# Kernel tuning notes

Hardware: AMD Instinct MI355X
Metric: run time of the kernel (lower is better)

## Reference

```python
import jax, jax.numpy as jnp
import numpy as np

N_NODES = 50000
N_EDGES = 800000
IN_FEATS = 128
OUT_FEATS = 128


def setup_inputs() -> dict:
    key = jax.random.key(0)
    k1, k2, k3, k4, k5 = jax.random.split(key, 5)
    feat = jax.random.normal(k1, (N_NODES, IN_FEATS), dtype=jnp.float32)
    src = jax.random.randint(k2, (N_EDGES,), 0, N_NODES, dtype=jnp.int64)
    dst = jax.random.randint(k3, (N_EDGES,), 0, N_NODES, dtype=jnp.int64)
    # Glorot uniform weight, zero bias (as in reset_parameters)
    limit = float(np.sqrt(6.0 / (IN_FEATS + OUT_FEATS)))
    weight = jax.random.uniform(k4, (IN_FEATS, OUT_FEATS), dtype=jnp.float32,
                                minval=-limit, maxval=limit)
    bias = jnp.zeros((OUT_FEATS,), dtype=jnp.float32)
    return {"feat": feat, "src": src, "dst": dst, "weight": weight, "bias": bias}


def reference(feat, src, dst, weight, bias):
    ones = jnp.ones(src.shape[0], dtype=feat.dtype)
    # out-degree normalization on source side
    deg_out = jnp.maximum(jax.ops.segment_sum(ones, src, num_segments=N_NODES), 1.0)
    h = feat * (deg_out ** -0.5)[:, None]  # [N, in]
    # in_feats <= out_feats: aggregate first, then matmul
    agg = jax.ops.segment_sum(h[src], dst, num_segments=N_NODES)  # SpMM: [N, in]
    rst = jnp.matmul(agg, weight)  # [N, out]
    # in-degree normalization on destination side
    deg_in = jnp.maximum(jax.ops.segment_sum(ones, dst, num_segments=N_NODES), 1.0)
    rst = rst * (deg_in ** -0.5)[:, None]
    rst = rst + bias
    return rst
```

## Files before the change

### kernel.cpp

```cpp
#include <hip/hip_runtime.h>

#define IN_F 128
#define HRH 4
#define HCD 64
#define HCS 32
#define HRB 8
#define HIST_RS 12544
#define BIN_RS 6272
#define LROW 68

typedef __attribute__((ext_vector_type(8))) short bf16x8;
typedef __attribute__((ext_vector_type(4))) float f32x4;

static __device__ __forceinline__ unsigned short f2bf(float x) {
    unsigned u = __float_as_uint(x);
    unsigned r = (u + 0x7FFFu + ((u >> 16) & 1u)) >> 16;
    return (unsigned short)r;
}

#define RFL(x) __builtin_amdgcn_readfirstlane(x)

__global__ __launch_bounds__(256) void k_hist(const int* __restrict__ src,
                                              const int* __restrict__ dst,
                                              int* __restrict__ dstpart,
                                              int* __restrict__ srcpart,
                                              int nN, int nE) {
    __shared__ int h[HIST_RS];
    int bid = blockIdx.x;
    const int* key;
    int* part;
    int r, c, nch;
    if (bid < HRH * HCD) {
        key = dst; part = dstpart; nch = HCD;
        r = bid / HCD; c = bid % HCD;
    } else {
        bid -= HRH * HCD;
        key = src; part = srcpart; nch = HCS;
        r = bid / HCS; c = bid % HCS;
    }
    const int rs   = (nN + HRH - 1) / HRH;
    const int rbeg = r * rs;
    const int rsize = min(rs, nN - rbeg);
    if (rsize <= 0) return;

    for (int i = threadIdx.x; i < rsize; i += 256) h[i] = 0;
    __syncthreads();

    const int chunk = (nE + nch - 1) / nch;
    const int ebeg = c * chunk;
    const int eend = min(ebeg + chunk, nE);

    if ((ebeg & 3) == 0) {
        for (int i = ebeg + threadIdx.x * 4; i < eend; i += 256 * 4) {
            if (i + 3 < eend) {
                const int4 k4 = *reinterpret_cast<const int4*>(key + i);
                int a;
                a = k4.x - rbeg; if ((unsigned)a < (unsigned)rsize) atomicAdd(&h[a], 1);
                a = k4.y - rbeg; if ((unsigned)a < (unsigned)rsize) atomicAdd(&h[a], 1);
                a = k4.z - rbeg; if ((unsigned)a < (unsigned)rsize) atomicAdd(&h[a], 1);
                a = k4.w - rbeg; if ((unsigned)a < (unsigned)rsize) atomicAdd(&h[a], 1);
            } else {
                for (int j = i; j < eend; ++j) {
                    int a = key[j] - rbeg;
                    if ((unsigned)a < (unsigned)rsize) atomicAdd(&h[a], 1);
                }
            }
        }
    } else {
        for (int i = ebeg + threadIdx.x; i < eend; i += 256) {
            int a = key[i] - rbeg;
            if ((unsigned)a < (unsigned)rsize) atomicAdd(&h[a], 1);
        }
    }
    __syncthreads();

    int* pout = part + (size_t)c * nN + rbeg;
    for (int i = threadIdx.x; i < rsize; i += 256) pout[i] = h[i];
}

__global__ void k_merge(int* __restrict__ dstpart, const int* __restrict__ srcpart,
                        int* __restrict__ cnt_pad, int* __restrict__ creal,
                        float* __restrict__ dinv_out, float* __restrict__ dinv_in,
                        int nN) {
    const int n = blockIdx.x * blockDim.x + threadIdx.x;
    if (n > nN) return;
    if (n == nN) { cnt_pad[n] = 0; return; }
    int s = 0;
#pragma unroll 4
    for (int c = 0; c < HCS; ++c) s += srcpart[(size_t)c * nN + n];
    int run = 0;
#pragma unroll 4
    for (int c = 0; c < HCD; ++c) {
        const size_t idx = (size_t)c * nN + n;
        int v = dstpart[idx];
        dstpart[idx] = run;
        run += v;
    }
    cnt_pad[n]  = (run + 7) & ~7;
    creal[n]    = run;
    dinv_out[n] = rsqrtf(fmaxf((float)s, 1.0f));
    dinv_in[n]  = rsqrtf(fmaxf((float)run, 1.0f));
}

__global__ __launch_bounds__(256) void k_scan_blk(const int* __restrict__ cnt,
                                                  int* __restrict__ offs,
                                                  int* __restrict__ part, int nNs) {
    __shared__ int ts[256];
    const int t = threadIdx.x;
    const int base = blockIdx.x * 1024 + t * 4;
    int4 v = make_int4(0, 0, 0, 0);
    if (base + 3 < nNs) {
        v = *reinterpret_cast<const int4*>(cnt + base);
    } else {
        if (base + 0 < nNs) v.x = cnt[base + 0];
        if (base + 1 < nNs) v.y = cnt[base + 1];
        if (base + 2 < nNs) v.z = cnt[base + 2];
        if (base + 3 < nNs) v.w = cnt[base + 3];
    }
    const int s = v.x + v.y + v.z + v.w;
    ts[t] = s;
    __syncthreads();
    for (int d = 1; d < 256; d <<= 1) {
        int u = (t >= d) ? ts[t - d] : 0;
        __syncthreads();
        ts[t] += u;
        __syncthreads();
    }
    const int ex = ts[t] - s;
    if (t == 255) part[blockIdx.x] = ts[255];
    int4 o;
    o.x = ex;
    o.y = o.x + v.x;
    o.z = o.y + v.y;
    o.w = o.z + v.z;
    if (base + 3 < nNs) {
        *reinterpret_cast<int4*>(offs + base) = o;
    } else {
        if (base + 0 < nNs) offs[base + 0] = o.x;
        if (base + 1 < nNs) offs[base + 1] = o.y;
        if (base + 2 < nNs) offs[base + 2] = o.z;
        if (base + 3 < nNs) offs[base + 3] = o.w;
    }
}

__global__ __launch_bounds__(256) void k_scan_top(int* __restrict__ part, int nb) {
    __shared__ int ts[256];
    const int t = threadIdx.x;
    const int v = (t < nb) ? part[t] : 0;
    ts[t] = v;
    __syncthreads();
    for (int d = 1; d < 256; d <<= 1) {
        int u = (t >= d) ? ts[t - d] : 0;
        __syncthreads();
        ts[t] += u;
        __syncthreads();
    }
    if (t < nb) part[t] = ts[t] - v;
}

__global__ __launch_bounds__(256) void k_scan_add(int* __restrict__ offs,
                                                  const int* __restrict__ part,
                                                  int nNs) {
    const int base = blockIdx.x * 1024 + threadIdx.x * 4;
    const int add = part[blockIdx.x];
    if (base + 3 < nNs) {
        int4 o = *reinterpret_cast<int4*>(offs + base);
        o.x += add; o.y += add; o.z += add; o.w += add;
        *reinterpret_cast<int4*>(offs + base) = o;
    } else {
#pragma unroll
        for (int j = 0; j < 4; ++j)
            if (base + j < nNs) offs[base + j] += add;
    }
}

__global__ void k_pad(const int* __restrict__ offs, const int* __restrict__ creal,
                      int* __restrict__ eidx, int nN) {
    const int n = blockIdx.x * blockDim.x + threadIdx.x;
    if (n >= nN) return;
    const int s = offs[n] + creal[n];
    const int e = offs[n + 1];
    for (int i = s; i < e; ++i) eidx[i] = nN;
}

__global__ __launch_bounds__(256) void k_bin2(const int* __restrict__ src,
                                              const int* __restrict__ dst,
                                              const int* __restrict__ offs,
                                              const int* __restrict__ chunkoff,
                                              int* __restrict__ eidx, int nN, int nE) {
    __shared__ int cur[BIN_RS];
    const int bid = blockIdx.x;
    const int r = bid / HCD;
    const int c = bid % HCD;
    const int rs = (nN + HRB - 1) / HRB;
    const int rbeg = r * rs;
    const int rsize = min(rs, nN - rbeg);
    if (rsize <= 0) return;

    for (int i = threadIdx.x; i < rsize; i += 256)
        cur[i] = offs[rbeg + i] + chunkoff[(size_t)c * nN + rbeg + i];
    __syncthreads();

    const int chunk = (nE + HCD - 1) / HCD;
    const int ebeg = c * chunk;
    const int eend = min(ebeg + chunk, nE);
    for (int i = ebeg + threadIdx.x * 4; i < eend; i += 256 * 4) {
        if (i + 3 < eend) {
            const int4 d4 = *reinterpret_cast<const int4*>(dst + i);
            int d;
            d = d4.x - rbeg; if ((unsigned)d < (unsigned)rsize) { int p = atomicAdd(&cur[d], 1); eidx[p] = src[i + 0]; }
            d = d4.y - rbeg; if ((unsigned)d < (unsigned)rsize) { int p = atomicAdd(&cur[d], 1); eidx[p] = src[i + 1]; }
            d = d4.z - rbeg; if ((unsigned)d < (unsigned)rsize) { int p = atomicAdd(&cur[d], 1); eidx[p] = src[i + 2]; }
            d = d4.w - rbeg; if ((unsigned)d < (unsigned)rsize) { int p = atomicAdd(&cur[d], 1); eidx[p] = src[i + 3]; }
        } else {
            for (int j = i; j < eend; ++j) {
                int d = dst[j] - rbeg;
                if ((unsigned)d < (unsigned)rsize) { int p = atomicAdd(&cur[d], 1); eidx[p] = src[j]; }
            }
        }
    }
}

__global__ __launch_bounds__(256) void k_scale(const float* __restrict__ feat,
                                               const float* __restrict__ dinv,
                                               unsigned short* __restrict__ h, int nN) {
    const int i = blockIdx.x * 256 + threadIdx.x;
    if (i >= (nN + 1) * (IN_F / 4)) return;
    const int node = i >> 5;
    const int j = (i & 31) * 4;
    ushort4 o = make_ushort4(0, 0, 0, 0);
    if (node < nN) {
        const float s = dinv[node];
        const float4 v = *reinterpret_cast<const float4*>(feat + (size_t)node * IN_F + j);
        o.x = f2bf(v.x * s);
        o.y = f2bf(v.y * s);
        o.z = f2bf(v.z * s);
        o.w = f2bf(v.w * s);
    }
    *reinterpret_cast<ushort4*>(h + (size_t)node * IN_F + j) = o;
}

__global__ __launch_bounds__(256) void k_wprep(const float* __restrict__ W,
                                               unsigned short* __restrict__ wt) {
    __shared__ float wl[128 * 128];
    for (int i = threadIdx.x * 4; i < 128 * 128; i += 256 * 4)
        *reinterpret_cast<float4*>(&wl[i]) = *reinterpret_cast<const float4*>(&W[i]);
    __syncthreads();
    const int col = threadIdx.x >> 1;
    const int k0  = (threadIdx.x & 1) * 64;
    for (int k = k0; k < k0 + 64; ++k)
        wt[col * 128 + k] = f2bf(wl[k * 128 + col]);
}

#define ISSUE8(vv, a0, a1)                                                        \
    vv##0 = *reinterpret_cast<const unsigned*>(h + (size_t)RFL(a0.x) * IN_F + lo); \
    vv##1 = *reinterpret_cast<const unsigned*>(h + (size_t)RFL(a0.y) * IN_F + lo); \
    vv##2 = *reinterpret_cast<const unsigned*>(h + (size_t)RFL(a0.z) * IN_F + lo); \
    vv##3 = *reinterpret_cast<const unsigned*>(h + (size_t)RFL(a0.w) * IN_F + lo); \
    vv##4 = *reinterpret_cast<const unsigned*>(h + (size_t)RFL(a1.x) * IN_F + lo); \
    vv##5 = *reinterpret_cast<const unsigned*>(h + (size_t)RFL(a1.y) * IN_F + lo); \
    vv##6 = *reinterpret_cast<const unsigned*>(h + (size_t)RFL(a1.z) * IN_F + lo); \
    vv##7 = *reinterpret_cast<const unsigned*>(h + (size_t)RFL(a1.w) * IN_F + lo);

#define ACC8(vv, ax, ay)                                                      \
    ax += __uint_as_float(vv##0 << 16); ay += __uint_as_float(vv##0 & 0xFFFF0000u); \
    ax += __uint_as_float(vv##1 << 16); ay += __uint_as_float(vv##1 & 0xFFFF0000u); \
    ax += __uint_as_float(vv##2 << 16); ay += __uint_as_float(vv##2 & 0xFFFF0000u); \
    ax += __uint_as_float(vv##3 << 16); ay += __uint_as_float(vv##3 & 0xFFFF0000u); \
    ax += __uint_as_float(vv##4 << 16); ay += __uint_as_float(vv##4 & 0xFFFF0000u); \
    ax += __uint_as_float(vv##5 << 16); ay += __uint_as_float(vv##5 & 0xFFFF0000u); \
    ax += __uint_as_float(vv##6 << 16); ay += __uint_as_float(vv##6 & 0xFFFF0000u); \
    ax += __uint_as_float(vv##7 << 16); ay += __uint_as_float(vv##7 & 0xFFFF0000u);

__global__ __launch_bounds__(256) void k_gg(
    const unsigned short* __restrict__ h, const int* __restrict__ eidx,
    const int* __restrict__ offs, const unsigned short* __restrict__ wt,
    const float* __restrict__ bias, const float* __restrict__ dinv_in,
    float* __restrict__ out, int nN) {
    __shared__ unsigned tile[16 * LROW];
    const int lane = threadIdx.x & 63;
    const int wave = threadIdx.x >> 6;
    const int blk16 = blockIdx.x * 16;
    const size_t lo = (size_t)(lane * 2);
    const int nbase = blk16 + wave * 4;

#pragma unroll
    for (int p = 0; p < 2; ++p) {
        const int rA = nbase + 2 * p;
        const int rB = rA + 1;
        int begA = 0, endA = 0, begB = 0, endB = 0;
        if (rA < nN) { begA = RFL(offs[rA]); endA = RFL(offs[rA + 1]); }
        if (rB < nN) { begB = RFL(offs[rB]); endB = RFL(offs[rB + 1]); }

        float axA = 0.f, ayA = 0.f, axB = 0.f, ayB = 0.f;
        int iA = begA, iB = begB;
        int4 a0, a1, b0, b1;
        bool lA = iA < endA, lB = iB < endB;
        if (lA) { a0 = *reinterpret_cast<const int4*>(eidx + RFL(iA));
                  a1 = *reinterpret_cast<const int4*>(eidx + RFL(iA) + 4); }
        if (lB) { b0 = *reinterpret_cast<const int4*>(eidx + RFL(iB));
                  b1 = *reinterpret_cast<const int4*>(eidx + RFL(iB) + 4); }

        while (lA | lB) {
            unsigned vA0, vA1, vA2, vA3, vA4, vA5, vA6, vA7;
            unsigned vB0, vB1, vB2, vB3, vB4, vB5, vB6, vB7;
            if (lA) { ISSUE8(vA, a0, a1) }
            if (lB) { ISSUE8(vB, b0, b1) }
            if (iA + 8 < endA) { a0 = *reinterpret_cast<const int4*>(eidx + RFL(iA) + 8);
                                 a1 = *reinterpret_cast<const int4*>(eidx + RFL(iA) + 12); }
            if (iB + 8 < endB) { b0 = *reinterpret_cast<const int4*>(eidx + RFL(iB) + 8);
                                 b1 = *reinterpret_cast<const int4*>(eidx + RFL(iB) + 12); }
            if (lA) { ACC8(vA, axA, ayA) iA += 8; }
            if (lB) { ACC8(vB, axB, ayB) iB += 8; }
            lA = iA < endA; lB = iB < endB;
        }

        tile[(wave * 4 + 2 * p + 0) * LROW + lane] = ((unsigned)f2bf(ayA) << 16) | (unsigned)f2bf(axA);
        tile[(wave * 4 + 2 * p + 1) * LROW + lane] = ((unsigned)f2bf(ayB) << 16) | (unsigned)f2bf(axB);
    }
    __syncthreads();

    const int g = lane >> 4;
    const int cl = lane & 15;

    float di[4];
#pragma unroll
    for (int q = 0; q < 4; ++q)
        di[q] = dinv_in[min(blk16 + g * 4 + q, nN - 1)];

    f32x4 acc0 = (f32x4){0.f, 0.f, 0.f, 0.f};
    f32x4 acc1 = (f32x4){0.f, 0.f, 0.f, 0.f};
    const int col0 = wave * 16 + cl;
    const int col1 = (wave + 4) * 16 + cl;

#pragma unroll
    for (int s = 0; s < 4; ++s) {
        const bf16x8 a = *reinterpret_cast<const bf16x8*>(tile + cl * LROW + s * 16 + g * 4);
        const bf16x8 b0 = *reinterpret_cast<const bf16x8*>(wt + (size_t)col0 * IN_F + s * 32 + g * 8);
        const bf16x8 b1 = *reinterpret_cast<const bf16x8*>(wt + (size_t)col1 * IN_F + s * 32 + g * 8);
        acc0 = __builtin_amdgcn_mfma_f32_16x16x32_bf16(a, b0, acc0, 0, 0, 0);
        acc1 = __builtin_amdgcn_mfma_f32_16x16x32_bf16(a, b1, acc1, 0, 0, 0);
    }

    const float bv0 = bias[col0];
    const float bv1 = bias[col1];
#pragma unroll
    for (int q = 0; q < 4; ++q) {
        const int rr = blk16 + g * 4 + q;
        if (rr < nN) {
            out[(size_t)rr * IN_F + col0] = acc0[q] * di[q] + bv0;
            out[(size_t)rr * IN_F + col1] = acc1[q] * di[q] + bv1;
        }
    }
}

extern "C" void kernel_launch(void* const* d_in, const int* in_sizes, int n_in,
                              void* d_out, int out_size, void* d_ws, size_t ws_size,
                              hipStream_t stream) {
    const float* feat = (const float*)d_in[0];
    const int*   src  = (const int*)d_in[1];
    const int*   dst  = (const int*)d_in[2];
    const float* W    = (const float*)d_in[3];
    const float* bias = (const float*)d_in[4];
    float*       out  = (float*)d_out;

    const int nE = in_sizes[1];
    const int nN = in_sizes[0] / IN_F;
    const int nNs = nN + 1;
    const int nb = (nNs + 1023) / 1024;

    char* base = (char*)d_ws;
    int*            dstpart  = (int*)base;
    int*            srcpart  = (int*)(base + (size_t)HCD * nN * 4);
    unsigned short* h        = (unsigned short*)base;
    int*            eidx     = (int*)(base + (size_t)(HCD + HCS) * nN * 4);
    int*            eidx_end = eidx + nE + 8 * nN;
    unsigned short* wt       = (unsigned short*)eidx_end;
    int*            cnt_pad  = (int*)(wt + 128 * 128);
    int*            creal    = cnt_pad + nNs + 4;
    float*          dinv_out = (float*)(creal + nN + 4);
    float*          dinv_in  = dinv_out + nN;
    int*            offs     = (int*)(dinv_in + nN);
    int*            partscan = offs + nNs + 4;

    k_hist    <<<HRH * (HCD + HCS), 256, 0, stream>>>(src, dst, dstpart, srcpart, nN, nE);
    k_merge   <<<(nNs + 255) / 256, 256, 0, stream>>>(dstpart, srcpart, cnt_pad, creal, dinv_out, dinv_in, nN);
    k_scan_blk<<<nb, 256, 0, stream>>>(cnt_pad, offs, partscan, nNs);
    k_scan_top<<<1, 256, 0, stream>>>(partscan, nb);
    k_scan_add<<<nb, 256, 0, stream>>>(offs, partscan, nNs);
    k_pad     <<<(nN + 255) / 256, 256, 0, stream>>>(offs, creal, eidx, nN);
    k_bin2    <<<HRB * HCD, 256, 0, stream>>>(src, dst, offs, dstpart, eidx, nN, nE);
    k_scale   <<<((nN + 1) * (IN_F / 4) + 255) / 256, 256, 0, stream>>>(feat, dinv_out, h, nN);
    k_wprep   <<<1, 256, 0, stream>>>(W, wt);
    k_gg      <<<(nN + 15) / 16, 256, 0, stream>>>(h, eidx, offs, wt, bias, dinv_in, out, nN);
}
```

Before: 124.0 us.

## Replace multi-kernel prefix scan with wave-level scan and atomic cursor; fuse prep kernels

The three-kernel global exclusive scan is replaced by a per-wave shuffle scan inside k_merge that reserves space with an atomicAdd on a global cursor. Node segments end up in arbitrary order rather than sorted, so segment ends come from offs plus cnt_pad instead of offs[n+1]. The padding fill, feature scaling and weight transpose are merged into a single k_prep launch. This cuts the launch count from ten to five and removes the serialized scan passes, at the cost of non-deterministic segment placement, which may reduce locality in the gather.

```diff
diff --git a/kernel.cpp b/kernel.cpp
--- a/kernel.cpp
+++ b/kernel.cpp
@@ -24,8 +24,10 @@
                                               const int* __restrict__ dst,
                                               int* __restrict__ dstpart,
                                               int* __restrict__ srcpart,
+                                              int* __restrict__ cursor,
                                               int nN, int nE) {
     __shared__ int h[HIST_RS];
+    if (blockIdx.x == 0 && threadIdx.x == 0) *cursor = 0;
     int bid = blockIdx.x;
     const int* key;
     int* part;
@@ -78,109 +80,43 @@
     for (int i = threadIdx.x; i < rsize; i += 256) pout[i] = h[i];
 }
 
-__global__ void k_merge(int* __restrict__ dstpart, const int* __restrict__ srcpart,
-                        int* __restrict__ cnt_pad, int* __restrict__ creal,
-                        float* __restrict__ dinv_out, float* __restrict__ dinv_in,
-                        int nN) {
+__global__ __launch_bounds__(256) void k_merge(
+    int* __restrict__ dstpart, const int* __restrict__ srcpart,
+    int* __restrict__ cnt_pad, int* __restrict__ creal, int* __restrict__ offs,
+    float* __restrict__ dinv_out, float* __restrict__ dinv_in,
+    int* __restrict__ cursor, int nN) {
     const int n = blockIdx.x * blockDim.x + threadIdx.x;
-    if (n > nN) return;
-    if (n == nN) { cnt_pad[n] = 0; return; }
-    int s = 0;
+    const int lane = threadIdx.x & 63;
+    int s = 0, run = 0;
+    if (n < nN) {
 #pragma unroll 4
-    for (int c = 0; c < HCS; ++c) s += srcpart[(size_t)c * nN + n];
-    int run = 0;
+        for (int c = 0; c < HCS; ++c) s += srcpart[(size_t)c * nN + n];
 #pragma unroll 4
-    for (int c = 0; c < HCD; ++c) {
-        const size_t idx = (size_t)c * nN + n;
-        int v = dstpart[idx];
-        dstpart[idx] = run;
-        run += v;
-    }
-    cnt_pad[n]  = (run + 7) & ~7;
-    creal[n]    = run;
-    dinv_out[n] = rsqrtf(fmaxf((float)s, 1.0f));
-    dinv_in[n]  = rsqrtf(fmaxf((float)run, 1.0f));
-}
-
-__global__ __launch_bounds__(256) void k_scan_blk(const int* __restrict__ cnt,
-                                                  int* __restrict__ offs,
-                                                  int* __restrict__ part, int nNs) {
-    __shared__ int ts[256];
-    const int t = threadIdx.x;
-    const int base = blockIdx.x * 1024 + t * 4;
-    int4 v = make_int4(0, 0, 0, 0);
-    if (base + 3 < nNs) {
-        v = *reinterpret_cast<const int4*>(cnt + base);
-    } else {
-        if (base + 0 < nNs) v.x = cnt[base + 0];
-        if (base + 1 < nNs) v.y = cnt[base + 1];
-        if (base + 2 < nNs) v.z = cnt[base + 2];
-        if (base + 3 < nNs) v.w = cnt[base + 3];
-    }
-    const int s = v.x + v.y + v.z + v.w;
-    ts[t] = s;
-    __syncthreads();
-    for (int d = 1; d < 256; d <<= 1) {
-        int u = (t >= d) ? ts[t - d] : 0;
-        __syncthreads();
-        ts[t] += u;
-        __syncthreads();
-    }
-    const int ex = ts[t] - s;
-    if (t == 255) part[blockIdx.x] = ts[255];
-    int4 o;
-    o.x = ex;
-    o.y = o.x + v.x;
-    o.z = o.y + v.y;
-    o.w = o.z + v.z;
-    if (base + 3 < nNs) {
-        *reinterpret_cast<int4*>(offs + base) = o;
-    } else {
-        if (base + 0 < nNs) offs[base + 0] = o.x;
-        if (base + 1 < nNs) offs[base + 1] = o.y;
-        if (base + 2 < nNs) offs[base + 2] = o.z;
-        if (base + 3 < nNs) offs[base + 3] = o.w;
-    }
-}
-
-__global__ __launch_bounds__(256) void k_scan_top(int* __restrict__ part, int nb) {
-    __shared__ int ts[256];
-    const int t = threadIdx.x;
-    const int v = (t < nb) ? part[t] : 0;
-    ts[t] = v;
-    __syncthreads();
-    for (int d = 1; d < 256; d <<= 1) {
-        int u = (t >= d) ? ts[t - d] : 0;
-        __syncthreads();
-        ts[t] += u;
-        __syncthreads();
-    }
-    if (t < nb) part[t] = ts[t] - v;
-}
-
-__global__ __launch_bounds__(256) void k_scan_add(int* __restrict__ offs,
-                                                  const int* __restrict__ part,
-                                                  int nNs) {
-    const int base = blockIdx.x * 1024 + threadIdx.x * 4;
-    const int add = part[blockIdx.x];
-    if (base + 3 < nNs) {
-        int4 o = *reinterpret_cast<int4*>(offs + base);
-        o.x += add; o.y += add; o.z += add; o.w += add;
-        *reinterpret_cast<int4*>(offs + base) = o;
-    } else {
-#pragma unroll
-        for (int j = 0; j < 4; ++j)
-            if (base + j < nNs) offs[base + j] += add;
-    }
-}
-
-__global__ void k_pad(const int* __restrict__ offs, const int* __restrict__ creal,
-                      int* __restrict__ eidx, int nN) {
-    const int n = blockIdx.x * blockDim.x + threadIdx.x;
-    if (n >= nN) return;
-    const int s = offs[n] + creal[n];
-    const int e = offs[n + 1];
-    for (int i = s; i < e; ++i) eidx[i] = nN;
+        for (int c = 0; c < HCD; ++c) {
+            const size_t idx = (size_t)c * nN + n;
+            int v = dstpart[idx];
+            dstpart[idx] = run;
+            run += v;
+        }
+    }
+    const int padded = (n < nN) ? ((run + 7) & ~7) : 0;
+    int x = padded;
+#pragma unroll
+    for (int d = 1; d < 64; d <<= 1) {
+        int y = __shfl_up(x, d);
+        if (lane >= d) x += y;
+    }
+    const int total = __shfl(x, 63);
+    int base = 0;
+    if (lane == 63 && total > 0) base = atomicAdd(cursor, total);
+    base = __shfl(base, 63);
+    if (n < nN) {
+        offs[n]     = base + x - padded;
+        cnt_pad[n]  = padded;
+        creal[n]    = run;
+        dinv_out[n] = rsqrtf(fmaxf((float)s, 1.0f));
+        dinv_in[n]  = rsqrtf(fmaxf((float)run, 1.0f));
+    }
 }
 
 __global__ __launch_bounds__(256) void k_bin2(const int* __restrict__ src,
@@ -221,35 +157,43 @@
     }
 }
 
-__global__ __launch_bounds__(256) void k_scale(const float* __restrict__ feat,
-                                               const float* __restrict__ dinv,
-                                               unsigned short* __restrict__ h, int nN) {
-    const int i = blockIdx.x * 256 + threadIdx.x;
-    if (i >= (nN + 1) * (IN_F / 4)) return;
-    const int node = i >> 5;
-    const int j = (i & 31) * 4;
-    ushort4 o = make_ushort4(0, 0, 0, 0);
-    if (node < nN) {
-        const float s = dinv[node];
-        const float4 v = *reinterpret_cast<const float4*>(feat + (size_t)node * IN_F + j);
-        o.x = f2bf(v.x * s);
-        o.y = f2bf(v.y * s);
-        o.z = f2bf(v.z * s);
-        o.w = f2bf(v.w * s);
-    }
-    *reinterpret_cast<ushort4*>(h + (size_t)node * IN_F + j) = o;
-}
-
-__global__ __launch_bounds__(256) void k_wprep(const float* __restrict__ W,
-                                               unsigned short* __restrict__ wt) {
-    __shared__ float wl[128 * 128];
-    for (int i = threadIdx.x * 4; i < 128 * 128; i += 256 * 4)
-        *reinterpret_cast<float4*>(&wl[i]) = *reinterpret_cast<const float4*>(&W[i]);
-    __syncthreads();
-    const int col = threadIdx.x >> 1;
-    const int k0  = (threadIdx.x & 1) * 64;
-    for (int k = k0; k < k0 + 64; ++k)
-        wt[col * 128 + k] = f2bf(wl[k * 128 + col]);
+__global__ __launch_bounds__(256) void k_prep(
+    const float* __restrict__ feat, const float* __restrict__ dinv,
+    unsigned short* __restrict__ h,
+    const int* __restrict__ offs, const int* __restrict__ creal,
+    const int* __restrict__ cnt_pad, int* __restrict__ eidx,
+    const float* __restrict__ W, unsigned short* __restrict__ wt,
+    int nN, int SB, int PB) {
+    const int b = blockIdx.x;
+    if (b < SB) {
+        const int i = b * 256 + threadIdx.x;
+        if (i >= (nN + 1) * (IN_F / 4)) return;
+        const int node = i >> 5;
+        const int j = (i & 31) * 4;
+        ushort4 o = make_ushort4(0, 0, 0, 0);
+        if (node < nN) {
+            const float s = dinv[node];
+            const float4 v = *reinterpret_cast<const float4*>(feat + (size_t)node * IN_F + j);
+            o.x = f2bf(v.x * s);
+            o.y = f2bf(v.y * s);
+            o.z = f2bf(v.z * s);
+            o.w = f2bf(v.w * s);
+        }
+        *reinterpret_cast<ushort4*>(h + (size_t)node * IN_F + j) = o;
+    } else if (b < SB + PB) {
+        const int n = (b - SB) * 256 + threadIdx.x;
+        if (n >= nN) return;
+        const int base = offs[n];
+        const int st = base + creal[n];
+        const int e  = base + cnt_pad[n];
+        for (int i = st; i < e; ++i) eidx[i] = nN;
+    } else {
+        const int t = (b - SB - PB) * 256 + threadIdx.x;
+        if (t >= 128 * 128) return;
+        const int col = t >> 7;
+        const int k = t & 127;
+        wt[col * 128 + k] = f2bf(W[k * 128 + col]);
+    }
 }
 
 #define ISSUE8(vv, a0, a1)                                                        \
@@ -262,7 +206,7 @@
     vv##6 = *reinterpret_cast<const unsigned*>(h + (size_t)RFL(a1.z) * IN_F + lo); \
     vv##7 = *reinterpret_cast<const unsigned*>(h + (size_t)RFL(a1.w) * IN_F + lo);
 
-#define ACC8(vv, ax, ay)                                                      \
+#define ACC8(vv, ax, ay)                                                            \
     ax += __uint_as_float(vv##0 << 16); ay += __uint_as_float(vv##0 & 0xFFFF0000u); \
     ax += __uint_as_float(vv##1 << 16); ay += __uint_as_float(vv##1 & 0xFFFF0000u); \
     ax += __uint_as_float(vv##2 << 16); ay += __uint_as_float(vv##2 & 0xFFFF0000u); \
@@ -274,7 +218,8 @@
 
 __global__ __launch_bounds__(256) void k_gg(
     const unsigned short* __restrict__ h, const int* __restrict__ eidx,
-    const int* __restrict__ offs, const unsigned short* __restrict__ wt,
+    const int* __restrict__ offs, const int* __restrict__ cnt_pad,
+    const unsigned short* __restrict__ wt,
     const float* __restrict__ bias, const float* __restrict__ dinv_in,
     float* __restrict__ out, int nN) {
     __shared__ unsigned tile[16 * LROW];
@@ -289,8 +234,8 @@
         const int rA = nbase + 2 * p;
         const int rB = rA + 1;
         int begA = 0, endA = 0, begB = 0, endB = 0;
-        if (rA < nN) { begA = RFL(offs[rA]); endA = RFL(offs[rA + 1]); }
-        if (rB < nN) { begB = RFL(offs[rB]); endB = RFL(offs[rB + 1]); }
+        if (rA < nN) { begA = RFL(offs[rA]); endA = begA + RFL(cnt_pad[rA]); }
+        if (rB < nN) { begB = RFL(offs[rB]); endB = begB + RFL(cnt_pad[rB]); }
 
         float axA = 0.f, ayA = 0.f, axB = 0.f, ayB = 0.f;
         int iA = begA, iB = begB;
@@ -366,8 +311,6 @@
 
     const int nE = in_sizes[1];
     const int nN = in_sizes[0] / IN_F;
-    const int nNs = nN + 1;
-    const int nb = (nNs + 1023) / 1024;
 
     char* base = (char*)d_ws;
     int*            dstpart  = (int*)base;
@@ -377,20 +320,21 @@
     int*            eidx_end = eidx + nE + 8 * nN;
     unsigned short* wt       = (unsigned short*)eidx_end;
     int*            cnt_pad  = (int*)(wt + 128 * 128);
-    int*            creal    = cnt_pad + nNs + 4;
+    int*            creal    = cnt_pad + nN + 4;
     float*          dinv_out = (float*)(creal + nN + 4);
     float*          dinv_in  = dinv_out + nN;
     int*            offs     = (int*)(dinv_in + nN);
-    int*            partscan = offs + nNs + 4;
-
-    k_hist    <<<HRH * (HCD + HCS), 256, 0, stream>>>(src, dst, dstpart, srcpart, nN, nE);
-    k_merge   <<<(nNs + 255) / 256, 256, 0, stream>>>(dstpart, srcpart, cnt_pad, creal, dinv_out, dinv_in, nN);
-    k_scan_blk<<<nb, 256, 0, stream>>>(cnt_pad, offs, partscan, nNs);
-    k_scan_top<<<1, 256, 0, stream>>>(partscan, nb);
-    k_scan_add<<<nb, 256, 0, stream>>>(offs, partscan, nNs);
-    k_pad     <<<(nN + 255) / 256, 256, 0, stream>>>(offs, creal, eidx, nN);
-    k_bin2    <<<HRB * HCD, 256, 0, stream>>>(src, dst, offs, dstpart, eidx, nN, nE);
-    k_scale   <<<((nN + 1) * (IN_F / 4) + 255) / 256, 256, 0, stream>>>(feat, dinv_out, h, nN);
-    k_wprep   <<<1, 256, 0, stream>>>(W, wt);
-    k_gg      <<<(nN + 15) / 16, 256, 0, stream>>>(h, eidx, offs, wt, bias, dinv_in, out, nN);
-}
+    int*            cursor   = offs + nN + 4;
+
+    const int SB = ((nN + 1) * (IN_F / 4) + 255) / 256;
+    const int PB = (nN + 255) / 256;
+    const int WB = (128 * 128 + 255) / 256;
+
+    k_hist <<<HRH * (HCD + HCS), 256, 0, stream>>>(src, dst, dstpart, srcpart, cursor, nN, nE);
+    k_merge<<<(nN + 255) / 256, 256, 0, stream>>>(dstpart, srcpart, cnt_pad, creal, offs,
+                                                  dinv_out, dinv_in, cursor, nN);
+    k_bin2 <<<HRB * HCD, 256, 0, stream>>>(src, dst, offs, dstpart, eidx, nN, nE);
+    k_prep <<<SB + PB + WB, 256, 0, stream>>>(feat, dinv_out, h, offs, creal, cnt_pad,
+                                              eidx, W, wt, nN, SB, PB);
+    k_gg   <<<(nN + 15) / 16, 256, 0, stream>>>(h, eidx, offs, cnt_pad, wt, bias, dinv_in, out, nN);
+}
```

After: 119.4 us. -3.7%, faster.
